# Kernel optimization log

Hardware: AMD Instinct MI355X
Metric: run time of the kernel (lower is better)

## Reference

```python
import math
import jax, jax.numpy as jnp
import numpy as np

B_SZ, N_TOK, D_INNER, S_STATE = 4, 1024, 384, 16
DT_MAX = 0.15


def setup_inputs() -> dict:
    key = jax.random.key(0)
    ks = jax.random.split(key, 10)
    dt_init = math.log(math.exp(0.1) - 1.0)  # softplus^-1(0.1)
    x = jax.random.normal(ks[0], (B_SZ, N_TOK, D_INNER), dtype=jnp.float32)
    dt_self_W = jax.random.uniform(ks[1], (D_INNER, D_INNER), minval=-1e-4, maxval=1e-4)
    dt_self_b = jnp.full((D_INNER,), dt_init, dtype=jnp.float32)
    dt_diff_W = jax.random.uniform(ks[2], (D_INNER, D_INNER), minval=-1e-4, maxval=1e-4)
    dt_diff_b = jnp.full((D_INNER,), dt_init, dtype=jnp.float32)
    B_W = jax.random.normal(ks[3], (D_INNER, S_STATE)) / math.sqrt(D_INNER)
    C_real_W = jax.random.normal(ks[4], (D_INNER, S_STATE)) / math.sqrt(D_INNER)
    C_imag_W = jax.random.normal(ks[5], (D_INNER, S_STATE)) / math.sqrt(D_INNER)
    D_param = jnp.ones((D_INNER,), dtype=jnp.float32)
    A_log = jnp.broadcast_to(jnp.log(jnp.arange(1, S_STATE + 1, dtype=jnp.float32))[None, :], (D_INNER, S_STATE))
    lap = jnp.array([[0.0, 1.0, 0.0], [1.0, -4.0, 1.0], [0.0, 1.0, 0.0]], dtype=jnp.float32) * 0.1
    conv_w = jnp.broadcast_to(lap[None, None], (D_INNER, 1, 3, 3)) + 0.01 * jax.random.normal(ks[6], (D_INNER, 1, 3, 3))
    reaction_alpha = 0.01 * jax.random.normal(ks[7], (1, 1, D_INNER, 1))
    reaction_beta = 0.01 * jax.random.normal(ks[8], (1, 1, D_INNER, 1))
    return {
        'x': x, 'dt_self_W': dt_self_W, 'dt_self_b': dt_self_b,
        'dt_diff_W': dt_diff_W, 'dt_diff_b': dt_diff_b,
        'B_W': B_W, 'C_real_W': C_real_W, 'C_imag_W': C_imag_W,
        'D_param': D_param, 'A_log': A_log, 'conv_w': conv_w,
        'reaction_alpha': reaction_alpha, 'reaction_beta': reaction_beta,
        'K_steps': 2,
    }


def _laplacian(h, conv_w, H, W):
    # h: (B, N, D, S) -> depthwise 3x3 conv with replicate pad over the HxW grid
    B, N, D, S = h.shape
    hs = h.transpose(0, 3, 2, 1).reshape(B * S, D, H, W)
    hp = jnp.pad(hs, ((0, 0), (0, 0), (1, 1), (1, 1)), mode='edge')
    lap = jax.lax.conv_general_dilated(
        hp, conv_w, window_strides=(1, 1), padding='VALID',
        feature_group_count=D, dimension_numbers=('NCHW', 'OIHW', 'NCHW'))
    return lap.reshape(B, S, D, N).transpose(0, 3, 2, 1)


def reference(x, dt_self_W, dt_self_b, dt_diff_W, dt_diff_b, B_W, C_real_W,
              C_imag_W, D_param, A_log, conv_w, reaction_alpha, reaction_beta,
              K_steps):
    B, N, D = x.shape
    H = Wg = int(math.sqrt(N))
    A = -jax.nn.softplus(A_log)  # (D, S)
    delta_s = jnp.minimum(jax.nn.softplus(x @ dt_self_W.T + dt_self_b), DT_MAX)[..., None]
    delta_d = jnp.minimum(jax.nn.softplus(x @ dt_diff_W.T + dt_diff_b), DT_MAX)[..., None]
    B_mat = x @ B_W          # (B, N, S)
    C_real = x @ C_real_W    # (B, N, S)
    C_imag = x @ C_imag_W    # (B, N, S)
    mamba_input = jnp.einsum('bnd,bns->bnds', x, B_mat)
    h_real = mamba_input
    h_imag = jnp.zeros_like(h_real)
    dt = 1.0 / K_steps
    A_exp = A[None, None]  # (1,1,D,S)
    for _ in range(K_steps):
        f1_real = delta_s * (A_exp * h_real + mamba_input)
        f1_imag = delta_s * (A_exp * h_imag)
        lap_real = _laplacian(h_real, conv_w, H, Wg)
        lap_imag = _laplacian(h_imag, conv_w, H, Wg)
        f2_real = delta_d * -lap_imag
        f2_imag = delta_d * lap_real
        reaction_scale = reaction_alpha - reaction_beta * (h_real ** 2 + h_imag ** 2)
        h_real = h_real + dt * (f1_real + f2_real + h_real * reaction_scale)
        h_imag = h_imag + dt * (f1_imag + f2_imag + h_imag * reaction_scale)
    y = (jnp.einsum('bnds,bns->bnd', h_real, C_real)
         + jnp.einsum('bnds,bns->bnd', h_imag, C_imag)
         + x * D_param)
    return y
```

## Files before the change

kernel.cpp:

```cpp
#include <hip/hip_runtime.h>
#include <hip/hip_fp16.h>
#include <math.h>

#define B_SZ    4
#define N_TOKC  1024
#define D_INNER 384
#define S_STATE 16
#define DT_MAX_V 0.15f
#define PLANE   (B_SZ * N_TOKC)
#define DN      ((size_t)B_SZ * D_INNER * N_TOKC)

typedef __attribute__((ext_vector_type(8))) short bf16x8;
typedef __attribute__((ext_vector_type(4))) float f32x4;

__device__ __forceinline__ float softplusf(float z) {
    return fmaxf(z, 0.f) + log1pf(expf(-fabsf(z)));
}

__device__ __forceinline__ unsigned short f2bf(float f) {
    unsigned u = __float_as_uint(f);
    unsigned r = (u + 0x7FFFu + ((u >> 16) & 1u)) >> 16;
    return (unsigned short)r;
}

__device__ __forceinline__ unsigned packh2(float a, float b) {
    __half2 h = __floats2half2_rn(a, b);
    union { __half2 h; unsigned u; } c; c.h = h; return c.u;
}
__device__ __forceinline__ __half2 uph2(unsigned u) {
    union { unsigned u; __half2 h; } c; c.u = u; return c.h;
}
__device__ __forceinline__ unsigned h2u(__half2 h) {
    union { __half2 h; unsigned u; } c; c.h = h; return c.u;
}

__device__ __forceinline__ size_t frag_off(int T, int kb, int q, int l16) {
    return ((size_t)((T * 12 + kb) * 4 + q)) * 128 + l16 * 8;
}

__device__ __forceinline__ bf16x8 pack8(const float* v) {
    bf16x8 o;
#pragma unroll
    for (int e = 0; e < 8; e++) o[e] = (short)f2bf(v[e]);
    return o;
}

__global__ __launch_bounds__(256) void k_prep(
    const float* __restrict__ x, const float* __restrict__ Ws, const float* __restrict__ Wd,
    const float* __restrict__ BW, const float* __restrict__ CrW, const float* __restrict__ CiW,
    const float* __restrict__ A_log,
    float* __restrict__ x_t, unsigned short* __restrict__ xp,
    unsigned short* __restrict__ Wdtp, unsigned short* __restrict__ Wbcp,
    float* __restrict__ A_tab)
{
    const int t = threadIdx.x;
    const int bx = blockIdx.x;
    if (bx < 1536) {
        __shared__ __align__(16) float tile[32][36];
        const int tok0 = (bx & 127) * 32;
        const int d0   = (bx >> 7) * 32;
        const int b = tok0 >> 10, n0 = tok0 & 1023;
        {
            const int r = t >> 3, c4 = (t & 7) * 4;
            const float4 v = *(const float4*)(x + (size_t)(tok0 + r) * D_INNER + d0 + c4);
            tile[r][c4 + 0] = v.x; tile[r][c4 + 1] = v.y;
            tile[r][c4 + 2] = v.z; tile[r][c4 + 3] = v.w;
        }
        __syncthreads();
        {
            const int dr = t >> 3, n4 = (t & 7) * 4;
            float4 o;
            o.x = tile[n4 + 0][dr]; o.y = tile[n4 + 1][dr];
            o.z = tile[n4 + 2][dr]; o.w = tile[n4 + 3][dr];
            *(float4*)(x_t + ((size_t)(b * D_INNER + d0 + dr)) * N_TOKC + n0 + n4) = o;
        }
        if (t < 128) {
            const int tt = t >> 6, q = (t >> 4) & 3, l16 = t & 15;
            const int row = tt * 16 + l16;
            float v[8];
#pragma unroll
            for (int e = 0; e < 8; e++) v[e] = tile[row][q * 8 + e];
            *(bf16x8*)(xp + frag_off((tok0 >> 4) + tt, d0 >> 5, q, l16)) = pack8(v);
        }
    } else if (bx < 1584) {
        const int vv = bx - 1536;
        const int mat = vv >= 24;
        const int dt16 = mat ? vv - 24 : vv;
        const float* W = mat ? Wd : Ws;
        unsigned short* dst = Wdtp + (size_t)mat * 147456;
#pragma unroll
        for (int it = 0; it < 3; it++) {
            const int item = t + it * 256;
            const int l16 = item & 15, q = (item >> 4) & 3, kb = item >> 6;
            const float* src = W + (size_t)(dt16 * 16 + l16) * D_INNER + kb * 32 + q * 8;
            float v[8];
            const float4 v0 = *(const float4*)(src);
            const float4 v1 = *(const float4*)(src + 4);
            v[0] = v0.x; v[1] = v0.y; v[2] = v0.z; v[3] = v0.w;
            v[4] = v1.x; v[5] = v1.y; v[6] = v1.z; v[7] = v1.w;
            *(bf16x8*)(dst + frag_off(dt16, kb, q, l16)) = pack8(v);
        }
    } else if (bx < 1587) {
        const int m = bx - 1584;
        const float* W2 = (m == 0) ? BW : ((m == 1) ? CrW : CiW);
#pragma unroll
        for (int it = 0; it < 3; it++) {
            const int item = t + it * 256;
            const int l16 = item & 15, q = (item >> 4) & 3, kb = item >> 6;
            float v[8];
#pragma unroll
            for (int e = 0; e < 8; e++)
                v[e] = W2[(size_t)(kb * 32 + q * 8 + e) * S_STATE + l16];
            *(bf16x8*)(Wbcp + (size_t)m * 6144 + frag_off(0, kb, q, l16)) = pack8(v);
        }
    } else {
        for (int i = t; i < D_INNER * S_STATE; i += 256)
            A_tab[i] = -softplusf(A_log[i]);
    }
}

__global__ __launch_bounds__(256) void k_gemm(
    const unsigned short* __restrict__ xp, const unsigned short* __restrict__ Wdtp,
    const unsigned short* __restrict__ Wbcp,
    const float* __restrict__ bs, const float* __restrict__ bd,
    unsigned* __restrict__ dsdd_t,
    unsigned* __restrict__ Bmp, uint2* __restrict__ crip)
{
    const int wave = threadIdx.x >> 6;
    const int lane = threadIdx.x & 63;
    const int quad = lane >> 4, l16 = lane & 15;

    if (blockIdx.x < 384) {
        const int dbase = (blockIdx.x >> 6) * 64;
        const int tbase = (blockIdx.x & 63) * 64;
        const int wd = (wave & 1) * 32;
        const int wt = (wave >> 1) * 32;
        const int dT0 = (dbase + wd) >> 4;
        const int tT0 = (tbase + wt) >> 4;

        f32x4 acc[2][2][2];
#pragma unroll
        for (int m = 0; m < 2; m++)
#pragma unroll
            for (int i = 0; i < 2; i++)
#pragma unroll
                for (int j = 0; j < 2; j++) acc[m][i][j] = (f32x4)0.f;

        bf16x8 a0[2][2], b0[2];
#pragma unroll
        for (int m = 0; m < 2; m++)
#pragma unroll
            for (int i = 0; i < 2; i++)
                a0[m][i] = *(const bf16x8*)(Wdtp + (size_t)m * 147456
                                            + frag_off(dT0 + i, 0, quad, l16));
#pragma unroll
        for (int j = 0; j < 2; j++)
            b0[j] = *(const bf16x8*)(xp + frag_off(tT0 + j, 0, quad, l16));

#pragma unroll 2
        for (int kb = 0; kb < 12; kb++) {
            bf16x8 a1[2][2], b1[2];
            const int kn = (kb < 11) ? kb + 1 : 11;
#pragma unroll
            for (int m = 0; m < 2; m++)
#pragma unroll
                for (int i = 0; i < 2; i++)
                    a1[m][i] = *(const bf16x8*)(Wdtp + (size_t)m * 147456
                                                + frag_off(dT0 + i, kn, quad, l16));
#pragma unroll
            for (int j = 0; j < 2; j++)
                b1[j] = *(const bf16x8*)(xp + frag_off(tT0 + j, kn, quad, l16));

#pragma unroll
            for (int m = 0; m < 2; m++)
#pragma unroll
                for (int i = 0; i < 2; i++)
#pragma unroll
                    for (int j = 0; j < 2; j++)
                        acc[m][i][j] = __builtin_amdgcn_mfma_f32_16x16x32_bf16(
                            a0[m][i], b0[j], acc[m][i][j], 0, 0, 0);

#pragma unroll
            for (int m = 0; m < 2; m++)
#pragma unroll
                for (int i = 0; i < 2; i++) a0[m][i] = a1[m][i];
#pragma unroll
            for (int j = 0; j < 2; j++) b0[j] = b1[j];
        }

#pragma unroll
        for (int i = 0; i < 2; i++)
#pragma unroll
            for (int j = 0; j < 2; j++) {
                const int tok = tbase + wt + j * 16 + l16;
                const int bb = tok >> 10, n = tok & 1023;
#pragma unroll
                for (int reg = 0; reg < 4; reg++) {
                    const int d = dbase + wd + i * 16 + quad * 4 + reg;
                    const float vs = fminf(softplusf(acc[0][i][j][reg] + bs[d]), DT_MAX_V);
                    const float vd = fminf(softplusf(acc[1][i][j][reg] + bd[d]), DT_MAX_V);
                    dsdd_t[((size_t)(bb * D_INNER + d)) * N_TOKC + n] = packh2(vs, vd);
                }
            }
    } else {
        const int tT = (blockIdx.x - 384) * 4 + wave;
        f32x4 acc[3];
#pragma unroll
        for (int m = 0; m < 3; m++) acc[m] = (f32x4)0.f;

#pragma unroll 1
        for (int kb = 0; kb < 12; kb++) {
            const bf16x8 b = *(const bf16x8*)(xp + frag_off(tT, kb, quad, l16));
#pragma unroll
            for (int m = 0; m < 3; m++) {
                const bf16x8 a = *(const bf16x8*)(Wbcp + (size_t)m * 6144
                                                  + frag_off(0, kb, quad, l16));
                acc[m] = __builtin_amdgcn_mfma_f32_16x16x32_bf16(a, b, acc[m], 0, 0, 0);
            }
        }

        const int tok = tT * 16 + l16;
#pragma unroll
        for (int pp = 0; pp < 2; pp++) {
            const int sp = quad * 2 + pp;
            const int re = pp * 2;
            Bmp[(size_t)sp * PLANE + tok] = packh2(acc[0][re], acc[0][re + 1]);
            uint2 cw2;
            cw2.x = packh2(acc[1][re],     acc[2][re]);
            cw2.y = packh2(acc[1][re + 1], acc[2][re + 1]);
            crip[(size_t)sp * PLANE + tok] = cw2;
        }
    }
}

#define PSTRIDE 33
#define PSIZE   (PSTRIDE * 32)

__global__ __launch_bounds__(256) void k_ssm(
    const float* __restrict__ x_t, const float* __restrict__ conv_w, const float* __restrict__ A_tab,
    const float* __restrict__ ralpha, const float* __restrict__ rbeta, const float* __restrict__ Dp,
    const unsigned* __restrict__ dsdd_t,
    const unsigned* __restrict__ Bmp, const uint2* __restrict__ crip,
    float* __restrict__ y_part)
{
    const int d  = blockIdx.x;
    const int b  = blockIdx.y;
    const int t  = threadIdx.x;
    const int c  = t & 31;
    const int g  = t >> 5;
    const int r0 = g * 4;

    __shared__ uint2 pl0[PSIZE];
    __shared__ uint2 pl1[2][PSIZE];

    __half2 wh[9];
#pragma unroll
    for (int i = 0; i < 9; i++) wh[i] = __float2half2_rn(conv_w[d * 9 + i]);
    const float alpha = ralpha[d];
    const float beta  = rbeta[d];
    const float Dv    = Dp[d];

    const size_t base_dn = ((size_t)(b * D_INNER + d)) * N_TOKC;
    const size_t base_sn = (size_t)b * N_TOKC;

    float xv[4], dsv[4], ddv[4];
    __half2 xvh[4];
#pragma unroll
    for (int k = 0; k < 4; k++) {
        const int n = (r0 + k) * 32 + c;
        xv[k] = x_t[base_dn + n];
        xvh[k] = __float2half2_rn(xv[k]);
        const __half2 dd = uph2(dsdd_t[base_dn + n]);
        dsv[k] = __low2float(dd);
        ddv[k] = __high2float(dd);
    }

    int tapw[6][3];
    {
        const int cm = (c > 0)  ? c - 1 : 0;
        const int cp = (c < 31) ? c + 1 : 31;
        const int rtop = (r0 > 0)  ? r0 - 1 : 0;
        const int rbot = (r0 < 28) ? r0 + 4 : 31;
        int rowb[6];
        rowb[0] = rtop * PSTRIDE;
#pragma unroll
        for (int k = 0; k < 4; k++) rowb[k + 1] = (r0 + k) * PSTRIDE;
        rowb[5] = rbot * PSTRIDE;
#pragma unroll
        for (int rr = 0; rr < 6; rr++) {
            tapw[rr][0] = rowb[rr] + cm;
            tapw[rr][1] = rowb[rr] + c;
            tapw[rr][2] = rowb[rr] + cp;
        }
    }
    const int ws0 = r0 * PSTRIDE + c;

    float yp[4] = { 0.f, 0.f, 0.f, 0.f };

#pragma unroll 1
    for (int sg = 0; sg < 4; sg++) {
        float A[4];
#pragma unroll
        for (int s = 0; s < 4; s++) A[s] = A_tab[d * S_STATE + sg * 4 + s];

        __half2 bmp[4][2];
#pragma unroll
        for (int k = 0; k < 4; k++) {
            const int n = (r0 + k) * 32 + c;
#pragma unroll
            for (int pp = 0; pp < 2; pp++)
                bmp[k][pp] = uph2(Bmp[(size_t)(sg * 2 + pp) * PLANE + base_sn + n]);
        }

#pragma unroll
        for (int k = 0; k < 4; k++) {
            const __half2 u01 = __hmul2(xvh[k], bmp[k][0]);
            const __half2 u23 = __hmul2(xvh[k], bmp[k][1]);
            pl0[ws0 + k * PSTRIDE] = make_uint2(h2u(u01), h2u(u23));
        }
        __syncthreads();

        {
            uint2 tp[6][3];
#pragma unroll
            for (int rr = 0; rr < 6; rr++)
#pragma unroll
                for (int j = 0; j < 3; j++)
                    tp[rr][j] = pl0[tapw[rr][j]];
#pragma unroll
            for (int k = 0; k < 4; k++) {
                __half2 ac01 = __float2half2_rn(0.f);
                __half2 ac23 = __float2half2_rn(0.f);
#pragma unroll
                for (int a = 0; a < 3; a++)
#pragma unroll
                    for (int j = 0; j < 3; j++) {
                        ac01 = __hfma2(wh[a * 3 + j], uph2(tp[k + a][j].x), ac01);
                        ac23 = __hfma2(wh[a * 3 + j], uph2(tp[k + a][j].y), ac23);
                    }
                const __half2 uc01 = uph2(tp[k + 1][1].x);
                const __half2 uc23 = uph2(tp[k + 1][1].y);
                const float uu[4]  = { __low2float(uc01), __high2float(uc01),
                                       __low2float(uc23), __high2float(uc23) };
                const float lap[4] = { __low2float(ac01), __high2float(ac01),
                                       __low2float(ac23), __high2float(ac23) };
                unsigned w[4];
#pragma unroll
                for (int s = 0; s < 4; s++) {
                    const float u   = uu[s];
                    const float f1r = dsv[k] * fmaf(A[s], u, u);
                    const float rs  = fmaf(-beta, u * u, alpha);
                    const float nhr = u + 0.5f * (f1r + u * rs);
                    const float nhi = 0.5f * ddv[k] * lap[s];
                    w[s] = packh2(nhr, nhi);
                }
                pl1[0][ws0 + k * PSTRIDE] = make_uint2(w[0], w[1]);
                pl1[1][ws0 + k * PSTRIDE] = make_uint2(w[2], w[3]);
            }
        }
        __syncthreads();

#pragma unroll
        for (int pp = 0; pp < 2; pp++) {
            uint2 cr2[4];
#pragma unroll
            for (int k = 0; k < 4; k++)
                cr2[k] = crip[(size_t)(sg * 2 + pp) * PLANE + base_sn + (r0 + k) * 32 + c];
            uint2 tp[6][3];
#pragma unroll
            for (int rr = 0; rr < 6; rr++)
#pragma unroll
                for (int j = 0; j < 3; j++)
                    tp[rr][j] = pl1[pp][tapw[rr][j]];
#pragma unroll
            for (int k = 0; k < 4; k++) {
                __half2 acE = __float2half2_rn(0.f);
                __half2 acO = __float2half2_rn(0.f);
#pragma unroll
                for (int a = 0; a < 3; a++)
#pragma unroll
                    for (int j = 0; j < 3; j++) {
                        acE = __hfma2(wh[a * 3 + j], uph2(tp[k + a][j].x), acE);
                        acO = __hfma2(wh[a * 3 + j], uph2(tp[k + a][j].y), acO);
                    }
                const __half2 hE = uph2(tp[k + 1][1].x);
                const __half2 hO = uph2(tp[k + 1][1].y);
#pragma unroll
                for (int e = 0; e < 2; e++) {
                    const int s = pp * 2 + e;
                    const __half2 hh = e ? hO : hE;
                    const __half2 ac = e ? acO : acE;
                    const float hrv  = __low2float(hh);
                    const float hiv  = __high2float(hh);
                    const float lapr = __low2float(ac);
                    const float lapi = __high2float(ac);
                    const float u    = xv[k] * (e ? __high2float(bmp[k][pp])
                                                  : __low2float(bmp[k][pp]));
                    const float f1r = dsv[k] * fmaf(A[s], hrv, u);
                    const float f1i = dsv[k] * (A[s] * hiv);
                    const float f2r = -ddv[k] * lapi;
                    const float f2i =  ddv[k] * lapr;
                    const float q   = fmaf(hrv, hrv, hiv * hiv);
                    const float rs  = fmaf(-beta, q, alpha);
                    const float nhr = hrv + 0.5f * (f1r + f2r + hrv * rs);
                    const float nhi = hiv + 0.5f * (f1i + f2i + hiv * rs);
                    const __half2 cri = uph2(e ? cr2[k].y : cr2[k].x);
                    yp[k] = fmaf(nhr, __low2float(cri), yp[k]);
                    yp[k] = fmaf(nhi, __high2float(cri), yp[k]);
                }
            }
        }
    }

#pragma unroll
    for (int k = 0; k < 4; k++)
        y_part[base_dn + (r0 + k) * 32 + c] = fmaf(xv[k], Dv, yp[k]);
}

__global__ __launch_bounds__(256) void k_reduce(
    const float* __restrict__ y_part, float* __restrict__ y)
{
    const int d0 = blockIdx.x * 32;
    const int n0 = blockIdx.y * 32;
    const int b  = blockIdx.z;
    const int t  = threadIdx.x;
    __shared__ __align__(16) float tile[32][36];

    const int dr = t >> 3, nc4 = (t & 7) * 4;
    const float4 v = *(const float4*)(y_part
        + ((size_t)(b * D_INNER + d0 + dr)) * N_TOKC + n0 + nc4);
    tile[dr][nc4 + 0] = v.x; tile[dr][nc4 + 1] = v.y;
    tile[dr][nc4 + 2] = v.z; tile[dr][nc4 + 3] = v.w;
    __syncthreads();

    const int nr = t >> 3, dc4 = (t & 7) * 4;
    float4 o;
    o.x = tile[dc4 + 0][nr];
    o.y = tile[dc4 + 1][nr];
    o.z = tile[dc4 + 2][nr];
    o.w = tile[dc4 + 3][nr];
    *(float4*)(y + ((size_t)(b * N_TOKC + n0 + nr)) * D_INNER + d0 + dc4) = o;
}

extern "C" void kernel_launch(void* const* d_in, const int* in_sizes, int n_in,
                              void* d_out, int out_size, void* d_ws, size_t ws_size,
                              hipStream_t stream)
{
    const float* x    = (const float*)d_in[0];
    const float* Ws   = (const float*)d_in[1];
    const float* bsb  = (const float*)d_in[2];
    const float* Wd   = (const float*)d_in[3];
    const float* bdb  = (const float*)d_in[4];
    const float* BW   = (const float*)d_in[5];
    const float* CrW  = (const float*)d_in[6];
    const float* CiW  = (const float*)d_in[7];
    const float* Dp   = (const float*)d_in[8];
    const float* Alog = (const float*)d_in[9];
    const float* cw   = (const float*)d_in[10];
    const float* ra   = (const float*)d_in[11];
    const float* rb   = (const float*)d_in[12];
    float* y = (float*)d_out;

    float* ws = (float*)d_ws;
    unsigned* dsdd_t = (unsigned*)ws;
    float* x_t    = ws + DN;
    unsigned* Bmp = (unsigned*)(x_t + DN);
    uint2* crip   = (uint2*)(Bmp + (size_t)8 * PLANE);
    float* A_tab  = (float*)(crip + (size_t)8 * PLANE);
    float* y_part = A_tab + (size_t)D_INNER * S_STATE;

    unsigned short* xp   = (unsigned short*)(y_part + DN);
    unsigned short* Wdtp = xp + (size_t)256 * 12 * 4 * 128;
    unsigned short* Wbcp = Wdtp + (size_t)2 * 147456;

    k_prep<<<dim3(1588), 256, 0, stream>>>(x, Ws, Wd, BW, CrW, CiW, Alog,
                                           x_t, xp, Wdtp, Wbcp, A_tab);
    k_gemm<<<dim3(448), 256, 0, stream>>>(xp, Wdtp, Wbcp, bsb, bdb,
                                          dsdd_t, Bmp, crip);
    k_ssm<<<dim3(D_INNER, B_SZ), 256, 0, stream>>>(x_t, cw, A_tab, ra, rb, Dp,
                                                   dsdd_t, Bmp, crip, y_part);
    k_reduce<<<dim3(12, 32, 4), 256, 0, stream>>>(y_part, y);
}
```

Baseline: 159.9 us.

## Repack planes as real/imag pairs and run SSM update in packed half2 math

Changes the intermediate plane layout so each packed word holds two states' real parts and another holds their imaginary parts, instead of real/imag pairs per state. The C-projection packing is changed to match. With this layout, the pointwise Euler-step updates in both stages run as packed half2 arithmetic with pre-halved coefficients, replacing scalar fp32 math and half-to-float unpacking. This cuts VALU instruction count and conversions. It gives up fp32 precision in the reaction and update terms, which raises accuracy risk.

```diff
diff --git a/kernel.cpp b/kernel.cpp
--- a/kernel.cpp
+++ b/kernel.cpp
@@ -226,8 +226,8 @@
             const int re = pp * 2;
             Bmp[(size_t)sp * PLANE + tok] = packh2(acc[0][re], acc[0][re + 1]);
             uint2 cw2;
-            cw2.x = packh2(acc[1][re],     acc[2][re]);
-            cw2.y = packh2(acc[1][re + 1], acc[2][re + 1]);
+            cw2.x = packh2(acc[1][re], acc[1][re + 1]);
+            cw2.y = packh2(acc[2][re], acc[2][re + 1]);
             crip[(size_t)sp * PLANE + tok] = cw2;
         }
     }
@@ -259,20 +259,24 @@
     const float alpha = ralpha[d];
     const float beta  = rbeta[d];
     const float Dv    = Dp[d];
+    const __half2 alh2  = __float2half2_rn(0.5f * alpha);
+    const __half2 nbeh2 = __float2half2_rn(-0.5f * beta);
 
     const size_t base_dn = ((size_t)(b * D_INNER + d)) * N_TOKC;
     const size_t base_sn = (size_t)b * N_TOKC;
 
-    float xv[4], dsv[4], ddv[4];
-    __half2 xvh[4];
+    float xv[4];
+    __half2 xvh[4], dsh2[4], ddh2[4], nddh2[4];
 #pragma unroll
     for (int k = 0; k < 4; k++) {
         const int n = (r0 + k) * 32 + c;
         xv[k] = x_t[base_dn + n];
         xvh[k] = __float2half2_rn(xv[k]);
         const __half2 dd = uph2(dsdd_t[base_dn + n]);
-        dsv[k] = __low2float(dd);
-        ddv[k] = __high2float(dd);
+        const float dsv = __low2float(dd), ddv = __high2float(dd);
+        dsh2[k]  = __float2half2_rn(0.5f * dsv);
+        ddh2[k]  = __float2half2_rn(0.5f * ddv);
+        nddh2[k] = __float2half2_rn(-0.5f * ddv);
     }
 
     int tapw[6][3];
@@ -299,9 +303,14 @@
 
 #pragma unroll 1
     for (int sg = 0; sg < 4; sg++) {
-        float A[4];
-#pragma unroll
-        for (int s = 0; s < 4; s++) A[s] = A_tab[d * S_STATE + sg * 4 + s];
+        __half2 A2[2], Ap1[2];
+#pragma unroll
+        for (int pp = 0; pp < 2; pp++) {
+            const float a0 = A_tab[d * S_STATE + sg * 4 + 2 * pp];
+            const float a1 = A_tab[d * S_STATE + sg * 4 + 2 * pp + 1];
+            A2[pp]  = __floats2half2_rn(a0, a1);
+            Ap1[pp] = __floats2half2_rn(a0 + 1.f, a1 + 1.f);
+        }
 
         __half2 bmp[4][2];
 #pragma unroll
@@ -329,33 +338,27 @@
                     tp[rr][j] = pl0[tapw[rr][j]];
 #pragma unroll
             for (int k = 0; k < 4; k++) {
-                __half2 ac01 = __float2half2_rn(0.f);
-                __half2 ac23 = __float2half2_rn(0.f);
+                __half2 lap[2];
+                lap[0] = __float2half2_rn(0.f);
+                lap[1] = __float2half2_rn(0.f);
 #pragma unroll
                 for (int a = 0; a < 3; a++)
 #pragma unroll
                     for (int j = 0; j < 3; j++) {
-                        ac01 = __hfma2(wh[a * 3 + j], uph2(tp[k + a][j].x), ac01);
-                        ac23 = __hfma2(wh[a * 3 + j], uph2(tp[k + a][j].y), ac23);
+                        lap[0] = __hfma2(wh[a * 3 + j], uph2(tp[k + a][j].x), lap[0]);
+                        lap[1] = __hfma2(wh[a * 3 + j], uph2(tp[k + a][j].y), lap[1]);
                     }
-                const __half2 uc01 = uph2(tp[k + 1][1].x);
-                const __half2 uc23 = uph2(tp[k + 1][1].y);
-                const float uu[4]  = { __low2float(uc01), __high2float(uc01),
-                                       __low2float(uc23), __high2float(uc23) };
-                const float lap[4] = { __low2float(ac01), __high2float(ac01),
-                                       __low2float(ac23), __high2float(ac23) };
-                unsigned w[4];
-#pragma unroll
-                for (int s = 0; s < 4; s++) {
-                    const float u   = uu[s];
-                    const float f1r = dsv[k] * fmaf(A[s], u, u);
-                    const float rs  = fmaf(-beta, u * u, alpha);
-                    const float nhr = u + 0.5f * (f1r + u * rs);
-                    const float nhi = 0.5f * ddv[k] * lap[s];
-                    w[s] = packh2(nhr, nhi);
+#pragma unroll
+                for (int pp = 0; pp < 2; pp++) {
+                    const __half2 u2 = uph2(pp ? tp[k + 1][1].y : tp[k + 1][1].x);
+                    const __half2 q2  = __hmul2(u2, u2);
+                    const __half2 rs2 = __hfma2(nbeh2, q2, alh2);
+                    __half2 S = __hmul2(dsh2[k], __hmul2(u2, Ap1[pp]));
+                    S = __hfma2(u2, rs2, S);
+                    const __half2 nhr2 = __hadd2(u2, S);
+                    const __half2 nhi2 = __hmul2(ddh2[k], lap[pp]);
+                    pl1[pp][ws0 + k * PSTRIDE] = make_uint2(h2u(nhr2), h2u(nhi2));
                 }
-                pl1[0][ws0 + k * PSTRIDE] = make_uint2(w[0], w[1]);
-                pl1[1][ws0 + k * PSTRIDE] = make_uint2(w[2], w[3]);
             }
         }
         __syncthreads();
@@ -374,40 +377,31 @@
                     tp[rr][j] = pl1[pp][tapw[rr][j]];
 #pragma unroll
             for (int k = 0; k < 4; k++) {
-                __half2 acE = __float2half2_rn(0.f);
-                __half2 acO = __float2half2_rn(0.f);
+                __half2 acR = __float2half2_rn(0.f);
+                __half2 acI = __float2half2_rn(0.f);
 #pragma unroll
                 for (int a = 0; a < 3; a++)
 #pragma unroll
                     for (int j = 0; j < 3; j++) {
-                        acE = __hfma2(wh[a * 3 + j], uph2(tp[k + a][j].x), acE);
-                        acO = __hfma2(wh[a * 3 + j], uph2(tp[k + a][j].y), acO);
+                        acR = __hfma2(wh[a * 3 + j], uph2(tp[k + a][j].x), acR);
+                        acI = __hfma2(wh[a * 3 + j], uph2(tp[k + a][j].y), acI);
                     }
-                const __half2 hE = uph2(tp[k + 1][1].x);
-                const __half2 hO = uph2(tp[k + 1][1].y);
-#pragma unroll
-                for (int e = 0; e < 2; e++) {
-                    const int s = pp * 2 + e;
-                    const __half2 hh = e ? hO : hE;
-                    const __half2 ac = e ? acO : acE;
-                    const float hrv  = __low2float(hh);
-                    const float hiv  = __high2float(hh);
-                    const float lapr = __low2float(ac);
-                    const float lapi = __high2float(ac);
-                    const float u    = xv[k] * (e ? __high2float(bmp[k][pp])
-                                                  : __low2float(bmp[k][pp]));
-                    const float f1r = dsv[k] * fmaf(A[s], hrv, u);
-                    const float f1i = dsv[k] * (A[s] * hiv);
-                    const float f2r = -ddv[k] * lapi;
-                    const float f2i =  ddv[k] * lapr;
-                    const float q   = fmaf(hrv, hrv, hiv * hiv);
-                    const float rs  = fmaf(-beta, q, alpha);
-                    const float nhr = hrv + 0.5f * (f1r + f2r + hrv * rs);
-                    const float nhi = hiv + 0.5f * (f1i + f2i + hiv * rs);
-                    const __half2 cri = uph2(e ? cr2[k].y : cr2[k].x);
-                    yp[k] = fmaf(nhr, __low2float(cri), yp[k]);
-                    yp[k] = fmaf(nhi, __high2float(cri), yp[k]);
-                }
+                const __half2 hr2 = uph2(tp[k + 1][1].x);
+                const __half2 hi2 = uph2(tp[k + 1][1].y);
+                const __half2 u2  = __hmul2(xvh[k], bmp[k][pp]);
+                const __half2 q2  = __hfma2(hr2, hr2, __hmul2(hi2, hi2));
+                const __half2 rs2 = __hfma2(nbeh2, q2, alh2);
+                __half2 Sr = __hmul2(dsh2[k], __hfma2(A2[pp], hr2, u2));
+                Sr = __hfma2(nddh2[k], acI, Sr);
+                Sr = __hfma2(hr2, rs2, Sr);
+                const __half2 nhr2 = __hadd2(hr2, Sr);
+                __half2 Si = __hmul2(dsh2[k], __hmul2(A2[pp], hi2));
+                Si = __hfma2(ddh2[k], acR, Si);
+                Si = __hfma2(hi2, rs2, Si);
+                const __half2 nhi2 = __hadd2(hi2, Si);
+                __half2 p2 = __hmul2(nhr2, uph2(cr2[k].x));
+                p2 = __hfma2(nhi2, uph2(cr2[k].y), p2);
+                yp[k] += __low2float(p2) + __high2float(p2);
             }
         }
     }
```

Result: faster. 151.9 us (-5.0%).
